# Kernel optimization log

Hardware: AMD Instinct MI355X
Metric: run time of the kernel (lower is better)

## Reference

```python
import jax, jax.numpy as jnp
import numpy as np
import math

B, L, D, H, FACTOR = 4, 2048, 256, 8, 5
DH = D // H

def setup_inputs() -> dict:
    key = jax.random.key(0)
    ks = jax.random.split(key, 12)
    s = 1.0 / math.sqrt(D)
    return {
        "q": jax.random.normal(ks[0], (B, L, D), jnp.float32),
        "k": jax.random.normal(ks[1], (B, L, D), jnp.float32),
        "v": jax.random.normal(ks[2], (B, L, D), jnp.float32),
        "Wq": jax.random.normal(ks[3], (D, D), jnp.float32) * s,
        "bq": jax.random.normal(ks[4], (D,), jnp.float32) * s,
        "Wk": jax.random.normal(ks[5], (D, D), jnp.float32) * s,
        "bk": jax.random.normal(ks[6], (D,), jnp.float32) * s,
        "Wv": jax.random.normal(ks[7], (D, D), jnp.float32) * s,
        "bv": jax.random.normal(ks[8], (D,), jnp.float32) * s,
        "Wc": jax.random.normal(ks[9], (D, D), jnp.float32) * s,
        "bc": jax.random.normal(ks[10], (D,), jnp.float32) * s,
        "index_sample": jax.random.randint(ks[11], (L,), 0, L),  # U_part = min(5*L*ceil(log1p(L)), L) = L
    }

def reference(q, k, v, Wq, bq, Wk, bk, Wv, bv, Wc, bc, index_sample):
    # projections (torch Linear: x @ W^T + b)
    qp = q @ Wq.T + bq
    kp = k @ Wk.T + bk
    vp = v @ Wv.T + bv
    # NOTE: original reshapes q with a raw view (no transpose), k/v via split()
    q4 = qp.reshape(B, H, L, DH)                       # faithful to q.view(B, H, L, dh)
    k4 = kp.reshape(B, L, H, DH).transpose(0, 2, 1, 3)
    v4 = vp.reshape(B, L, H, DH).transpose(0, 2, 1, 3)
    qf = q4.reshape(B * H, L, DH)
    kf = k4.reshape(B * H, L, DH)
    vf = v4.reshape(B * H, L, DH)
    # random K sampling (with replacement); U_part == L here
    K_sample = kf[:, index_sample, :]                  # [BH, L, dh]
    QK = jnp.einsum('bld,bud->blu', qf, K_sample)      # [BH, L, L]
    M = QK.max(axis=-1) - QK.sum(axis=-1) / L          # sparsity measure [BH, L]
    u = min(FACTOR * math.ceil(math.log1p(L)), L)      # = 40
    _, top_idx = jax.lax.top_k(-M, u)                  # topk(..., largest=False)
    Q_red = jnp.take_along_axis(qf, top_idx[:, :, None], axis=1)  # [BH, u, dh]
    scores = jnp.einsum('bud,bld->bul', Q_red, kf) / math.sqrt(DH)
    probs = jax.nn.softmax(scores, axis=-1)
    out = jnp.einsum('bul,bld->bud', probs, vf)        # [BH, u, dh]
    out = out.reshape(B, H, u, DH).transpose(0, 2, 1, 3).reshape(B, u, D)
    return out @ Wc.T + bc
```

## Files before the change

kernel.cpp:

```cpp
#include <hip/hip_runtime.h>
#include <math.h>

#define B_ 4
#define L_ 2048
#define D_ 256
#define H_ 8
#define DH_ 32
#define NH_ 32
#define U_ 40
#define LD_ 524288
#define NCH_ 16

typedef __attribute__((ext_vector_type(8))) short short8;
typedef __attribute__((ext_vector_type(4))) float floatx4;

static __device__ __forceinline__ unsigned long long ullmin_(unsigned long long a, unsigned long long b) {
    return a < b ? a : b;
}
static __device__ __forceinline__ unsigned short f2bf_rne(float x) {
    unsigned u = __float_as_uint(x);
    unsigned r = u + 0x7FFFu + ((u >> 16) & 1u);
    return (unsigned short)(r >> 16);
}
static __device__ __forceinline__ float bf2f(unsigned short h) {
    return __uint_as_float(((unsigned)h) << 16);
}

__global__ __launch_bounds__(256) void wsplit(const float* __restrict__ Wq,
                                              const float* __restrict__ Wk,
                                              const float* __restrict__ Wv,
                                              unsigned short* __restrict__ Whs,
                                              unsigned short* __restrict__ Wms,
                                              unsigned short* __restrict__ Wls) {
    const int g = blockIdx.x * 256 + threadIdx.x;
    const int mat = g >> 14;
    const int rem = g & 16383;
    const int col = rem >> 6;
    const int k4 = rem & 63;
    const float* W = (mat == 0) ? Wq : (mat == 1) ? Wk : Wv;
    const float4 x = *(const float4*)(W + (size_t)col * 256 + k4 * 4);
    float xs[4] = {x.x, x.y, x.z, x.w};
    unsigned short hv[4], mv[4], lv[4];
#pragma unroll
    for (int j = 0; j < 4; ++j) {
        hv[j] = f2bf_rne(xs[j]);
        const float e1 = xs[j] - bf2f(hv[j]);
        mv[j] = f2bf_rne(e1);
        const float e2 = e1 - bf2f(mv[j]);
        lv[j] = f2bf_rne(e2);
    }
    const int colblk = col >> 6, c64 = col & 63;
    const int jt = c64 >> 4, cin = c64 & 15;
    const int kt = k4 >> 3, g8 = k4 & 7;
    const int quad = g8 >> 1, half = g8 & 1;
    const size_t o = ((((size_t)mat * 4 + colblk) * 8 + kt) << 11) +
                     jt * 512 + (quad * 16 + cin) * 8 + half * 4;
    *(ushort4*)(Whs + o) = make_ushort4(hv[0], hv[1], hv[2], hv[3]);
    *(ushort4*)(Wms + o) = make_ushort4(mv[0], mv[1], mv[2], mv[3]);
    *(ushort4*)(Wls + o) = make_ushort4(lv[0], lv[1], lv[2], lv[3]);
}

__global__ __launch_bounds__(256) void gemm_proj(const float* __restrict__ q,
                                                 const float* __restrict__ k,
                                                 const float* __restrict__ v,
                                                 const unsigned short* __restrict__ Whs,
                                                 const unsigned short* __restrict__ Wms,
                                                 const unsigned short* __restrict__ Wls,
                                                 const float* __restrict__ bq,
                                                 const float* __restrict__ bk,
                                                 const float* __restrict__ bv,
                                                 float* __restrict__ qp,
                                                 float* __restrict__ kp,
                                                 float* __restrict__ vp) {
    const int mat = blockIdx.z;
    const float* X = (mat == 0) ? q : (mat == 1) ? k : v;
    const float* bias = (mat == 0) ? bq : (mat == 1) ? bk : bv;
    float* Y = (mat == 0) ? qp : (mat == 1) ? kp : vp;
    const bool vmat = (mat == 2);

    const int t = threadIdx.x;
    const int w = t >> 6, lane = t & 63;
    const int lq = lane & 15, quad = lane >> 4;
    const int rowBase = blockIdx.x * 64 + w * 16;
    const int colBase = blockIdx.y * 128;
    const int nseg = vmat ? 16 : 24;

    __shared__ unsigned short Bls[2][12288];

    floatx4 acc[8];
#pragma unroll
    for (int nt2 = 0; nt2 < 8; ++nt2) acc[nt2] = (floatx4){0.f, 0.f, 0.f, 0.f};

    auto gsrc = [&](int s, int kt) -> const unsigned short* {
        const int p = s >> 3, rm = s & 7, chunk = rm >> 2, jj = rm & 3;
        const unsigned short* Wp = (p == 0) ? Whs : (p == 1) ? Wms : Wls;
        return Wp + (((((size_t)mat * 4 + ((blockIdx.y << 1) | chunk)) * 8 + kt) << 11) +
                     jj * 512 + lane * 8);
    };

#pragma unroll
    for (int n = 0; n < 6; ++n) {
        const int s = w + n * 4;
        if (s < nseg)
            *(short8*)&Bls[0][s * 512 + lane * 8] = *(const short8*)gsrc(s, 0);
    }
    __syncthreads();

    for (int kt = 0; kt < 8; ++kt) {
        const int buf = kt & 1;

        short8 stg[6];
#pragma unroll
        for (int n = 0; n < 6; ++n) {
            const int s = w + n * 4;
            if (kt < 7 && s < nseg) stg[n] = *(const short8*)gsrc(s, kt + 1);
        }

        short8 Ah, Am, Al;
        {
            const float* xr = X + (size_t)(rowBase + lq) * 256 + kt * 32 + quad * 8;
            const float4 x0 = *(const float4*)xr;
            const float4 x1 = *(const float4*)(xr + 4);
            float xs[8] = {x0.x, x0.y, x0.z, x0.w, x1.x, x1.y, x1.z, x1.w};
#pragma unroll
            for (int j = 0; j < 8; ++j) {
                const unsigned short h = f2bf_rne(xs[j]);
                const float e1 = xs[j] - bf2f(h);
                const unsigned short md = f2bf_rne(e1);
                Ah[j] = (short)h;
                Am[j] = (short)md;
                if (!vmat) {
                    const float e2 = e1 - bf2f(md);
                    Al[j] = (short)f2bf_rne(e2);
                }
            }
        }

        const unsigned short* Bb = Bls[buf];
#pragma unroll
        for (int nt2 = 0; nt2 < 8; ++nt2) {
            const int boff = ((nt2 >> 2) << 11) + ((nt2 & 3) << 9) + lane * 8;
            const short8 Bh = *(const short8*)&Bb[boff];
            const short8 Bm = *(const short8*)&Bb[4096 + boff];
            floatx4 a = acc[nt2];
            if (!vmat) {
                const short8 Bl = *(const short8*)&Bb[8192 + boff];
                a = __builtin_amdgcn_mfma_f32_16x16x32_bf16(Am, Bm, a, 0, 0, 0);
                a = __builtin_amdgcn_mfma_f32_16x16x32_bf16(Ah, Bl, a, 0, 0, 0);
                a = __builtin_amdgcn_mfma_f32_16x16x32_bf16(Al, Bh, a, 0, 0, 0);
                a = __builtin_amdgcn_mfma_f32_16x16x32_bf16(Ah, Bm, a, 0, 0, 0);
                a = __builtin_amdgcn_mfma_f32_16x16x32_bf16(Am, Bh, a, 0, 0, 0);
                a = __builtin_amdgcn_mfma_f32_16x16x32_bf16(Ah, Bh, a, 0, 0, 0);
            } else {
                a = __builtin_amdgcn_mfma_f32_16x16x32_bf16(Ah, Bm, a, 0, 0, 0);
                a = __builtin_amdgcn_mfma_f32_16x16x32_bf16(Am, Bh, a, 0, 0, 0);
                a = __builtin_amdgcn_mfma_f32_16x16x32_bf16(Ah, Bh, a, 0, 0, 0);
            }
            acc[nt2] = a;
        }

#pragma unroll
        for (int n = 0; n < 6; ++n) {
            const int s = w + n * 4;
            if (kt < 7 && s < nseg)
                *(short8*)&Bls[buf ^ 1][s * 512 + lane * 8] = stg[n];
        }
        __syncthreads();
    }

#pragma unroll
    for (int nt2 = 0; nt2 < 8; ++nt2) {
        const int c = colBase + nt2 * 16 + lq;
        const float bv_ = bias[c];
#pragma unroll
        for (int r = 0; r < 4; ++r) {
            const int mr = rowBase + quad * 4 + r;
            Y[(size_t)mr * 256 + c] = acc[nt2][r] + bv_;
        }
    }
}

__global__ __launch_bounds__(256) void kconv_ksum(const float* __restrict__ kp,
                                                  const int* __restrict__ idx,
                                                  unsigned short* __restrict__ Khi,
                                                  unsigned short* __restrict__ Klo,
                                                  float* __restrict__ Ksum32) {
    const int blk = ((blockIdx.x & 7) << 7) + (blockIdx.x >> 3);
    const int i = blk >> 5, uc = blk & 31;
    const int b = i >> 3, h = i & 7;
    const int t = threadIdx.x;
    const int dq = (t & 7) * 4;
    const int ur = t >> 3;

    __shared__ float part[32][36];
    float ksum[4] = {0.f, 0.f, 0.f, 0.f};

#pragma unroll
    for (int p = 0; p < 2; ++p) {
        int u = uc * 64 + p * 32 + ur;
        const float4 x = *(const float4*)(kp + (size_t)b * LD_ + (size_t)idx[u] * D_ + h * DH_ + dq);
        float xs[4] = {x.x, x.y, x.z, x.w};
        unsigned short hv[4], lv[4];
#pragma unroll
        for (int j = 0; j < 4; ++j) {
            ksum[j] += xs[j];
            hv[j] = f2bf_rne(xs[j]);
            lv[j] = f2bf_rne(xs[j] - bf2f(hv[j]));
        }
        size_t o = ((size_t)i * 2048 + u) * 32 + dq;
        *(ushort4*)(Khi + o) = make_ushort4(hv[0], hv[1], hv[2], hv[3]);
        *(ushort4*)(Klo + o) = make_ushort4(lv[0], lv[1], lv[2], lv[3]);
    }
#pragma unroll
    for (int j = 0; j < 4; ++j) part[ur][dq + j] = ksum[j];
    __syncthreads();
    if (t < 32) {
        float s = 0.f;
#pragma unroll 8
        for (int u2 = 0; u2 < 32; ++u2) s += part[u2][t];
        Ksum32[(size_t)blk * 32 + t] = s;
    }
}

__global__ __launch_bounds__(256) void mpart_mfma(const float* __restrict__ qp,
                                                  const unsigned short* __restrict__ Khi,
                                                  const unsigned short* __restrict__ Klo,
                                                  const float* __restrict__ Ksum32,
                                                  float* __restrict__ Mv,
                                                  float* __restrict__ Qmean) {
    const int lb = ((blockIdx.x & 7) << 6) + (blockIdx.x >> 3);
    const int i = lb >> 4;
    const int lg = lb & 15;
    const int t = threadIdx.x;
    const int w = t >> 6;
    const int lane = t & 63;
    const int lq = lane & 15;
    const int quad = lane >> 4;

    __shared__ float ssum[32];
    __shared__ float red[4][128];
    if (t < 32) {
        float s = 0.f;
#pragma unroll 8
        for (int uc = 0; uc < 32; ++uc) s += Ksum32[((size_t)i * 32 + uc) * 32 + t];
        ssum[t] = s;
    }

    short8 Ah[8], Al[8];
#pragma unroll
    for (int lt = 0; lt < 8; ++lt) {
        const int l = lg * 128 + lt * 16 + lq;
        const float* qrow = qp + ((size_t)i * 2048 + l) * 32 + quad * 8;
        float4 x0 = *(const float4*)(qrow);
        float4 x1 = *(const float4*)(qrow + 4);
        float xs[8] = {x0.x, x0.y, x0.z, x0.w, x1.x, x1.y, x1.z, x1.w};
#pragma unroll
        for (int j = 0; j < 8; ++j) {
            unsigned short h = f2bf_rne(xs[j]);
            unsigned short lo = f2bf_rne(xs[j] - bf2f(h));
            Ah[lt][j] = (short)h;
            Al[lt][j] = (short)lo;
        }
    }

    floatx4 rmax[8];
#pragma unroll
    for (int lt = 0; lt < 8; ++lt)
        rmax[lt] = (floatx4){-INFINITY, -INFINITY, -INFINITY, -INFINITY};

    const size_t kfrag = ((size_t)i * 2048 + w * 512 + lq) * 32 + quad * 8;
    const unsigned short* ph = Khi + kfrag;
    const unsigned short* pl = Klo + kfrag;
#pragma unroll 2
    for (int s = 0; s < 32; ++s) {
        short8 Bh = *(const short8*)(ph + (size_t)s * 512);
        short8 Bl = *(const short8*)(pl + (size_t)s * 512);
#pragma unroll
        for (int lt = 0; lt < 8; ++lt) {
            floatx4 acc = (floatx4){0.f, 0.f, 0.f, 0.f};
            acc = __builtin_amdgcn_mfma_f32_16x16x32_bf16(Al[lt], Bh, acc, 0, 0, 0);
            acc = __builtin_amdgcn_mfma_f32_16x16x32_bf16(Ah[lt], Bl, acc, 0, 0, 0);
            acc = __builtin_amdgcn_mfma_f32_16x16x32_bf16(Ah[lt], Bh, acc, 0, 0, 0);
#pragma unroll
            for (int r = 0; r < 4; ++r) rmax[lt][r] = fmaxf(rmax[lt][r], acc[r]);
        }
    }

#pragma unroll
    for (int lt = 0; lt < 8; ++lt)
#pragma unroll
        for (int r = 0; r < 4; ++r) {
            float v = rmax[lt][r];
#pragma unroll
            for (int off = 1; off < 16; off <<= 1)
                v = fmaxf(v, __shfl_xor(v, off, 64));
            rmax[lt][r] = v;
        }
    if (lq == 0) {
#pragma unroll
        for (int lt = 0; lt < 8; ++lt)
#pragma unroll
            for (int r = 0; r < 4; ++r)
                red[w][lt * 16 + quad * 4 + r] = rmax[lt][r];
    }
    __syncthreads();
    if (t < 128) {
        const int l = lg * 128 + t;
        float m = fmaxf(fmaxf(red[0][t], red[1][t]), fmaxf(red[2][t], red[3][t]));
        const float4* q4 = (const float4*)(qp + ((size_t)i * 2048 + l) * 32);
        const float4* s4 = (const float4*)ssum;
        float qs = 0.f;
#pragma unroll
        for (int z = 0; z < 8; ++z) {
            float4 a = q4[z];
            float4 c = s4[z];
            qs = fmaf(a.x, c.x, qs);
            qs = fmaf(a.y, c.y, qs);
            qs = fmaf(a.z, c.z, qs);
            qs = fmaf(a.w, c.w, qs);
        }
        const float qm = qs * (1.0f / 2048.0f);
        Qmean[(size_t)i * 2048 + l] = qm;
        Mv[(size_t)i * 2048 + l] = m - qm;
    }
}

__global__ __launch_bounds__(256) void topk64_fast(const float* __restrict__ Mv,
                                                   int* __restrict__ candIdx) {
    const int i = blockIdx.x;
    const int t = threadIdx.x;
    const int w = t >> 6, lane = t & 63;

    __shared__ unsigned hist[256];
    __shared__ unsigned sh_prefix, sh_selBelow;
    __shared__ unsigned cnt;
    __shared__ int candLds[64];
    __shared__ unsigned long long wred[4];

    unsigned v[8];
#pragma unroll
    for (int j = 0; j < 8; ++j) {
        const unsigned u = __float_as_uint(Mv[(size_t)i * 2048 + t + 256 * j]);
        v[j] = (u & 0x80000000u) ? ~u : (u | 0x80000000u);
    }

    if (t == 0) { sh_prefix = 0u; sh_selBelow = 0u; cnt = 0u; }

    for (int level = 0; level < 4; ++level) {
        const int shift = 24 - 8 * level;
        __syncthreads();
        const unsigned prefHi = sh_prefix;
        const unsigned selB = sh_selBelow;
        const unsigned mask = (level == 0) ? 0u : (0xFFFFFFFFu << (shift + 8));
        hist[t] = 0u;
        __syncthreads();
#pragma unroll
        for (int j = 0; j < 8; ++j)
            if ((v[j] & mask) == prefHi)
                atomicAdd(&hist[(v[j] >> shift) & 255u], 1u);
        __syncthreads();
        if (t < 64) {
            const unsigned c0 = hist[t * 4 + 0], c1 = hist[t * 4 + 1];
            const unsigned c2 = hist[t * 4 + 2], c3 = hist[t * 4 + 3];
            const unsigned i0 = c0, i1 = c0 + c1, i2 = i1 + c2, i3 = i2 + c3;
            unsigned x = i3;
#pragma unroll
            for (int off = 1; off < 64; off <<= 1) {
                const unsigned y = __shfl_up(x, off, 64);
                if (t >= off) x += y;
            }
            const unsigned excl = x - i3;
            const unsigned r = 64u - selB;
            const unsigned long long ball = __ballot(x >= r);
            const int flane = __ffsll(ball) - 1;
            if (t == flane) {
                unsigned k, ce;
                if (excl + i0 >= r)      { k = 0u; ce = excl; }
                else if (excl + i1 >= r) { k = 1u; ce = excl + i0; }
                else if (excl + i2 >= r) { k = 2u; ce = excl + i1; }
                else                     { k = 3u; ce = excl + i2; }
                sh_prefix = prefHi | (((unsigned)t * 4u + k) << shift);
                sh_selBelow = selB + ce;
            }
        }
    }
    __syncthreads();
    const unsigned thr = sh_prefix;
    const unsigned selB = sh_selBelow;
    const int rem = 64 - (int)selB;

    unsigned long long keys[8];
#pragma unroll
    for (int j = 0; j < 8; ++j) {
        const int l = t + 256 * j;
        if (v[j] < thr) {
            const unsigned p = atomicAdd(&cnt, 1u);
            candLds[p] = l;
            keys[j] = ~0ULL;
        } else if (v[j] == thr) {
            keys[j] = ((unsigned long long)v[j] << 32) | (unsigned)l;
        } else {
            keys[j] = ~0ULL;
        }
    }
    __syncthreads();

    for (int it = 0; it < rem; ++it) {
        unsigned long long best = keys[0];
#pragma unroll
        for (int j = 1; j < 8; ++j) best = ullmin_(best, keys[j]);
#pragma unroll
        for (int off = 1; off < 64; off <<= 1)
            best = ullmin_(best, __shfl_xor(best, off, 64));
        if (lane == 0) wred[w] = best;
        __syncthreads();
        const unsigned long long m = ullmin_(ullmin_(wred[0], wred[1]), ullmin_(wred[2], wred[3]));
        if (t == 0) candLds[selB + it] = (int)(m & 0xffffffffu);
#pragma unroll
        for (int j = 0; j < 8; ++j)
            if (keys[j] == m) keys[j] = ~0ULL;
        __syncthreads();
    }

    if (t < 64) candIdx[i * 64 + t] = candLds[t];
}

__global__ __launch_bounds__(256) void refine_kernel(const float* __restrict__ qp,
                                                     const float* __restrict__ kp,
                                                     const int* __restrict__ idx,
                                                     const int* __restrict__ candIdx,
                                                     float* __restrict__ refPart) {
    const int blk = blockIdx.x;
    const int i = blk >> 3, c = blk & 7;
    const int b = i >> 3, h = i & 7;
    const int t = threadIdx.x;
    __shared__ float qc[64][40];
    __shared__ float Ks[128][40];

    {
        const int cand = t >> 2, dp = (t & 3) * 8;
        const int l = candIdx[i * 64 + cand];
        const float* src = qp + ((size_t)i * 2048 + l) * 32 + dp;
        *(float4*)&qc[cand][dp] = *(const float4*)(src);
        *(float4*)&qc[cand][dp + 4] = *(const float4*)(src + 4);
    }
    __syncthreads();

    const int cand = t >> 2, usub = t & 3;
    float qv[32];
#pragma unroll
    for (int z = 0; z < 8; ++z) {
        float4 a = *(const float4*)&qc[cand][z * 4];
        qv[4 * z] = a.x; qv[4 * z + 1] = a.y; qv[4 * z + 2] = a.z; qv[4 * z + 3] = a.w;
    }

    float m = -INFINITY;
    for (int s = 0; s < 2; ++s) {
        {
            const int r = t >> 1, half = t & 1;
            const int u = c * 256 + s * 128 + r;
            const float* krow = kp + (size_t)b * LD_ + (size_t)idx[u] * D_ + h * DH_ + half * 16;
#pragma unroll
            for (int z = 0; z < 4; ++z)
                *(float4*)&Ks[r][half * 16 + z * 4] = *(const float4*)(krow + z * 4);
        }
        __syncthreads();
        for (int ur = usub; ur < 128; ur += 4) {
            float a0 = 0, a1 = 0, a2 = 0, a3 = 0;
#pragma unroll
            for (int z = 0; z < 8; ++z) {
                float4 kv = *(const float4*)&Ks[ur][z * 4];
                a0 = fmaf(qv[4 * z], kv.x, a0);
                a1 = fmaf(qv[4 * z + 1], kv.y, a1);
                a2 = fmaf(qv[4 * z + 2], kv.z, a2);
                a3 = fmaf(qv[4 * z + 3], kv.w, a3);
            }
            m = fmaxf(m, (a0 + a1) + (a2 + a3));
        }
        __syncthreads();
    }
    m = fmaxf(m, __shfl_xor(m, 1, 64));
    m = fmaxf(m, __shfl_xor(m, 2, 64));
    if ((t & 3) == 0) refPart[((size_t)i * 8 + c) * 64 + cand] = m;
}

#define SCP2 136
#define VSP 36

__global__ __launch_bounds__(320) void attn_part(const float* __restrict__ qp,
                                                 const float* __restrict__ kp,
                                                 const float* __restrict__ vp,
                                                 const int* __restrict__ candIdx,
                                                 const float* __restrict__ refPart,
                                                 const float* __restrict__ Qmean,
                                                 float* __restrict__ mPart,
                                                 float* __restrict__ sPart,
                                                 float* __restrict__ oPart) {
    const int blk = blockIdx.x;
    const int i = blk >> 4, c = blk & 15;
    const int b = i >> 3, h = i & 7;
    const int t = threadIdx.x;

    __shared__ float Qs[40][32];
    __shared__ float Vs[128][VSP];
    __shared__ float sc[40][SCP2];
    __shared__ float mred[40], sred[40];
    __shared__ int topl[40];

    if (t < 64) {
        const int l = candIdx[i * 64 + t];
        float m = -INFINITY;
#pragma unroll
        for (int cc = 0; cc < 8; ++cc) m = fmaxf(m, refPart[((size_t)i * 8 + cc) * 64 + t]);
        float Mex = m - Qmean[(size_t)i * 2048 + l];
        unsigned u32 = __float_as_uint(Mex);
        u32 = (u32 & 0x80000000u) ? ~u32 : (u32 | 0x80000000u);
        unsigned long long key = ((unsigned long long)u32 << 32) | (unsigned)l;
        for (int it = 0; it < 40; ++it) {
            unsigned long long k2 = key;
#pragma unroll
            for (int off = 1; off < 64; off <<= 1) k2 = ullmin_(k2, __shfl_xor(k2, off, 64));
            if (key == k2) {
                topl[it] = l;
                key = ~0ULL;
            }
        }
    } else {
        for (int e = t - 64; e < 1024; e += 256) {
            const int r = e >> 3, qq = e & 7;
            *(float4*)&Vs[r][qq * 4] =
                *(const float4*)(vp + (size_t)b * LD_ + (size_t)(c * 128 + r) * 256 + h * 32 + qq * 4);
        }
    }
    __syncthreads();

    {
        const int r = t >> 3, qq = t & 7;
        const int lq = topl[r];
        *(float4*)&Qs[r][qq * 4] = *(const float4*)(qp + ((size_t)i * 2048 + lq) * 32 + qq * 4);
    }
    __syncthreads();

    const float scale = 0.17677669529663687f;

    if (t < 256) {
        const int r = t >> 1;
        const int j0 = (t & 1) * 20;
        const float* kr = kp + (size_t)b * LD_ + (size_t)(c * 128 + r) * 256 + h * 32;
        float kv[32];
#pragma unroll
        for (int z = 0; z < 8; ++z) {
            float4 x = *(const float4*)(kr + z * 4);
            kv[4 * z] = x.x; kv[4 * z + 1] = x.y; kv[4 * z + 2] = x.z; kv[4 * z + 3] = x.w;
        }
#pragma unroll 4
        for (int jj = 0; jj < 20; ++jj) {
            const int j = j0 + jj;
            float a0 = 0, a1 = 0, a2 = 0, a3 = 0;
#pragma unroll
            for (int z = 0; z < 8; ++z) {
                const float4 q4 = *(const float4*)&Qs[j][z * 4];
                a0 = fmaf(kv[4 * z], q4.x, a0);
                a1 = fmaf(kv[4 * z + 1], q4.y, a1);
                a2 = fmaf(kv[4 * z + 2], q4.z, a2);
                a3 = fmaf(kv[4 * z + 3], q4.w, a3);
            }
            sc[j][r] = ((a0 + a1) + (a2 + a3)) * scale;
        }
    }
    __syncthreads();

    {
        const int w = t >> 6, lane = t & 63;
#pragma unroll
        for (int rr = 0; rr < 8; ++rr) {
            const int j = w * 8 + rr;
            float x0 = sc[j][lane], x1 = sc[j][lane + 64];
            float m = fmaxf(x0, x1);
#pragma unroll
            for (int off = 1; off < 64; off <<= 1) m = fmaxf(m, __shfl_xor(m, off, 64));
            const float e0 = __expf(x0 - m), e1 = __expf(x1 - m);
            sc[j][lane] = e0; sc[j][lane + 64] = e1;
            float s = e0 + e1;
#pragma unroll
            for (int off = 1; off < 64; off <<= 1) s += __shfl_xor(s, off, 64);
            if (lane == 0) { mred[j] = m; sred[j] = s; }
        }
    }
    __syncthreads();

    {
        const int j = t >> 3, qq = t & 7;
        float4 acc = make_float4(0.f, 0.f, 0.f, 0.f);
        for (int l = 0; l < 128; ++l) {
            const float p = sc[j][l];
            const float4 v4 = *(const float4*)&Vs[l][qq * 4];
            acc.x = fmaf(p, v4.x, acc.x);
            acc.y = fmaf(p, v4.y, acc.y);
            acc.z = fmaf(p, v4.z, acc.z);
            acc.w = fmaf(p, v4.w, acc.w);
        }
        const size_t o = (size_t)(i * NCH_ + c) * 40 + j;
        *(float4*)&oPart[o * 32 + qq * 4] = acc;
        if (qq == 0) { mPart[o] = mred[j]; sPart[o] = sred[j]; }
    }
}

__global__ __launch_bounds__(256) void attn_combine(const float* __restrict__ mPart,
                                                    const float* __restrict__ sPart,
                                                    const float* __restrict__ oPart,
                                                    float* __restrict__ attnOut) {
    const int blk = blockIdx.x;
    const int b = blk / 40, j = blk - b * 40;
    const int t = threadIdx.x;
    const int h = t >> 5, d = t & 31;
    const int i = b * 8 + h;

    float mv[NCH_];
    float M = -INFINITY;
#pragma unroll
    for (int c = 0; c < NCH_; ++c) {
        mv[c] = mPart[(size_t)(i * NCH_ + c) * 40 + j];
        M = fmaxf(M, mv[c]);
    }
    float S = 0.f, O = 0.f;
#pragma unroll
    for (int c = 0; c < NCH_; ++c) {
        const float sc_ = __expf(mv[c] - M);
        const size_t o = (size_t)(i * NCH_ + c) * 40 + j;
        S = fmaf(sPart[o], sc_, S);
        O = fmaf(oPart[o * 32 + d], sc_, O);
    }
    attnOut[((size_t)b * 40 + j) * 256 + h * 32 + d] = O / S;
}

__global__ __launch_bounds__(256) void gemm_out(const float* __restrict__ X,
                                                const float* __restrict__ Wc,
                                                const float* __restrict__ bias,
                                                float* __restrict__ Y) {
    const int t = threadIdx.x;
    const int rowBase = blockIdx.x * 16;
    const int colBase = blockIdx.y * 64;
    const int col = colBase + (t & 63);
    const int rq = (t >> 6) * 4;

    __shared__ float Xs[16][256];
#pragma unroll
    for (int e = t; e < 1024; e += 256) {
        const int r = e >> 6, kq = (e & 63) * 4;
        *(float4*)&Xs[r][kq] = *(const float4*)(X + (size_t)(rowBase + r) * 256 + kq);
    }
    __syncthreads();

    const float* wr = Wc + (size_t)col * 256;
    float acc[4] = {0.f, 0.f, 0.f, 0.f};
#pragma unroll 8
    for (int k = 0; k < 256; k += 4) {
        const float4 wv = *(const float4*)(wr + k);
#pragma unroll
        for (int r = 0; r < 4; ++r) {
            acc[r] = fmaf(Xs[rq + r][k + 0], wv.x, acc[r]);
            acc[r] = fmaf(Xs[rq + r][k + 1], wv.y, acc[r]);
            acc[r] = fmaf(Xs[rq + r][k + 2], wv.z, acc[r]);
            acc[r] = fmaf(Xs[rq + r][k + 3], wv.w, acc[r]);
        }
    }

    const float bv = bias[col];
#pragma unroll
    for (int r = 0; r < 4; ++r)
        Y[(size_t)(rowBase + rq + r) * 256 + col] = acc[r] + bv;
}

extern "C" void kernel_launch(void* const* d_in, const int* in_sizes, int n_in,
                              void* d_out, int out_size, void* d_ws, size_t ws_size,
                              hipStream_t stream) {
    const float* q  = (const float*)d_in[0];
    const float* k  = (const float*)d_in[1];
    const float* v  = (const float*)d_in[2];
    const float* Wq = (const float*)d_in[3];
    const float* bq = (const float*)d_in[4];
    const float* Wk = (const float*)d_in[5];
    const float* bk = (const float*)d_in[6];
    const float* Wv = (const float*)d_in[7];
    const float* bv = (const float*)d_in[8];
    const float* Wc = (const float*)d_in[9];
    const float* bc = (const float*)d_in[10];
    const int* idx  = (const int*)d_in[11];
    float* out = (float*)d_out;

    char* w = (char*)d_ws;
    float*          qp      = (float*)(w);
    float*          kp      = (float*)(w + (8u << 20));
    float*          vp      = (float*)(w + (16u << 20));
    unsigned short* Khi     = (unsigned short*)(w + (24u << 20));
    unsigned short* Klo     = (unsigned short*)(w + (28u << 20));
    float*          Mv      = (float*)(w + (32u << 20));
    float*          Qmean   = (float*)(w + (32u << 20) + (256u << 10));
    float*          Ksum32  = (float*)(w + (32u << 20) + (512u << 10));
    int*            candIdx = (int*)  (w + (32u << 20) + (640u << 10));
    float*          refPart = (float*)(w + (32u << 20) + (656u << 10));
    float*          attnOut = (float*)(w + (32u << 20) + (720u << 10));
    unsigned short* Whs     = (unsigned short*)(w + (40u << 20));
    unsigned short* Wms     = (unsigned short*)(w + (40u << 20) + (512u << 10));
    unsigned short* Wls     = (unsigned short*)(w + (41u << 20));
    float*          mPart   = (float*)(w + (24u << 20));
    float*          sPart   = (float*)(w + (24u << 20) + (128u << 10));
    float*          oPart   = (float*)(w + (24u << 20) + (256u << 10));

    hipLaunchKernelGGL(wsplit, dim3(192), dim3(256), 0, stream, Wq, Wk, Wv, Whs, Wms, Wls);
    hipLaunchKernelGGL(gemm_proj, dim3(128, 2, 3), dim3(256), 0, stream,
                       q, k, v, Whs, Wms, Wls, bq, bk, bv, qp, kp, vp);
    hipLaunchKernelGGL(kconv_ksum, dim3(1024), dim3(256), 0, stream, kp, idx, Khi, Klo, Ksum32);
    hipLaunchKernelGGL(mpart_mfma, dim3(512), dim3(256), 0, stream, qp, Khi, Klo, Ksum32, Mv, Qmean);
    hipLaunchKernelGGL(topk64_fast, dim3(32), dim3(256), 0, stream, Mv, candIdx);
    hipLaunchKernelGGL(refine_kernel, dim3(256), dim3(256), 0, stream, qp, kp, idx, candIdx, refPart);
    hipLaunchKernelGGL(attn_part, dim3(512), dim3(320), 0, stream,
                       qp, kp, vp, candIdx, refPart, Qmean, mPart, sPart, oPart);
    hipLaunchKernelGGL(attn_combine, dim3(160), dim3(256), 0, stream, mPart, sPart, oPart, attnOut);
    hipLaunchKernelGGL(gemm_out, dim3(10, 4), dim3(256), 0, stream, attnOut, Wc, bc, out);
}
```

Measured before the change: 213.7 us.

## Pre-split activations into bf16 hi/mid/lo tiles in a separate kernel

Adds an xsplit kernel that converts q/k/v into three bf16 components stored in an MFMA-fragment-friendly tiled layout. gemm_proj then loads these fragments directly and register-prefetches the next k-tile instead of converting fp32 inline, which removes the split arithmetic from the GEMM's critical path. The cost is an extra launch and roughly 1.5x the original activation bytes written and re-read through global memory (the three bf16 planes, with no lo plane for v), plus a larger workspace.

```diff
diff --git a/kernel.cpp b/kernel.cpp
--- a/kernel.cpp
+++ b/kernel.cpp
@@ -60,9 +60,43 @@
     *(ushort4*)(Wls + o) = make_ushort4(lv[0], lv[1], lv[2], lv[3]);
 }
 
-__global__ __launch_bounds__(256) void gemm_proj(const float* __restrict__ q,
-                                                 const float* __restrict__ k,
-                                                 const float* __restrict__ v,
+__global__ __launch_bounds__(256) void xsplit(const float* __restrict__ q,
+                                              const float* __restrict__ k,
+                                              const float* __restrict__ v,
+                                              unsigned short* __restrict__ Xh,
+                                              unsigned short* __restrict__ Xm,
+                                              unsigned short* __restrict__ Xl) {
+    const int g = blockIdx.x * 256 + threadIdx.x;
+    const int mat = g >> 19;
+    const int rem = g & 524287;
+    const int row = rem >> 6;
+    const int k4 = rem & 63;
+    const float* X = (mat == 0) ? q : (mat == 1) ? k : v;
+    const float4 x = *(const float4*)(X + (size_t)row * 256 + k4 * 4);
+    float xs[4] = {x.x, x.y, x.z, x.w};
+    unsigned short hv[4], mv[4], lv[4];
+#pragma unroll
+    for (int j = 0; j < 4; ++j) {
+        hv[j] = f2bf_rne(xs[j]);
+        const float e1 = xs[j] - bf2f(hv[j]);
+        mv[j] = f2bf_rne(e1);
+        const float e2 = e1 - bf2f(mv[j]);
+        lv[j] = f2bf_rne(e2);
+    }
+    const int rowtile = row >> 4, rin = row & 15;
+    const int kt = k4 >> 3, g8 = k4 & 7;
+    const int quad = g8 >> 1, half = g8 & 1;
+    const size_t o = ((((size_t)mat * 512 + rowtile) * 8 + kt) << 9) +
+                     (quad * 16 + rin) * 8 + half * 4;
+    *(ushort4*)(Xh + o) = make_ushort4(hv[0], hv[1], hv[2], hv[3]);
+    *(ushort4*)(Xm + o) = make_ushort4(mv[0], mv[1], mv[2], mv[3]);
+    if (mat < 2)
+        *(ushort4*)(Xl + o) = make_ushort4(lv[0], lv[1], lv[2], lv[3]);
+}
+
+__global__ __launch_bounds__(256) void gemm_proj(const unsigned short* __restrict__ Xh,
+                                                 const unsigned short* __restrict__ Xm,
+                                                 const unsigned short* __restrict__ Xl,
                                                  const unsigned short* __restrict__ Whs,
                                                  const unsigned short* __restrict__ Wms,
                                                  const unsigned short* __restrict__ Wls,
@@ -73,7 +107,6 @@
                                                  float* __restrict__ kp,
                                                  float* __restrict__ vp) {
     const int mat = blockIdx.z;
-    const float* X = (mat == 0) ? q : (mat == 1) ? k : v;
     const float* bias = (mat == 0) ? bq : (mat == 1) ? bk : bv;
     float* Y = (mat == 0) ? qp : (mat == 1) ? kp : vp;
     const bool vmat = (mat == 2);
@@ -84,6 +117,7 @@
     const int rowBase = blockIdx.x * 64 + w * 16;
     const int colBase = blockIdx.y * 128;
     const int nseg = vmat ? 16 : 24;
+    const int rowtile = blockIdx.x * 4 + w;
 
     __shared__ unsigned short Bls[2][12288];
 
@@ -97,6 +131,9 @@
         return Wp + (((((size_t)mat * 4 + ((blockIdx.y << 1) | chunk)) * 8 + kt) << 11) +
                      jj * 512 + lane * 8);
     };
+    auto abase = [&](int kt) -> size_t {
+        return ((((size_t)mat * 512 + rowtile) * 8 + kt) << 9) + lane * 8;
+    };
 
 #pragma unroll
     for (int n = 0; n < 6; ++n) {
@@ -104,35 +141,25 @@
         if (s < nseg)
             *(short8*)&Bls[0][s * 512 + lane * 8] = *(const short8*)gsrc(s, 0);
     }
+    short8 Ah = *(const short8*)(Xh + abase(0));
+    short8 Am = *(const short8*)(Xm + abase(0));
+    short8 Al;
+    if (!vmat) Al = *(const short8*)(Xl + abase(0));
     __syncthreads();
 
     for (int kt = 0; kt < 8; ++kt) {
         const int buf = kt & 1;
 
+        short8 nAh, nAm, nAl;
         short8 stg[6];
-#pragma unroll
-        for (int n = 0; n < 6; ++n) {
-            const int s = w + n * 4;
-            if (kt < 7 && s < nseg) stg[n] = *(const short8*)gsrc(s, kt + 1);
-        }
-
-        short8 Ah, Am, Al;
-        {
-            const float* xr = X + (size_t)(rowBase + lq) * 256 + kt * 32 + quad * 8;
-            const float4 x0 = *(const float4*)xr;
-            const float4 x1 = *(const float4*)(xr + 4);
-            float xs[8] = {x0.x, x0.y, x0.z, x0.w, x1.x, x1.y, x1.z, x1.w};
-#pragma unroll
-            for (int j = 0; j < 8; ++j) {
-                const unsigned short h = f2bf_rne(xs[j]);
-                const float e1 = xs[j] - bf2f(h);
-                const unsigned short md = f2bf_rne(e1);
-                Ah[j] = (short)h;
-                Am[j] = (short)md;
-                if (!vmat) {
-                    const float e2 = e1 - bf2f(md);
-                    Al[j] = (short)f2bf_rne(e2);
-                }
+        if (kt < 7) {
+            nAh = *(const short8*)(Xh + abase(kt + 1));
+            nAm = *(const short8*)(Xm + abase(kt + 1));
+            if (!vmat) nAl = *(const short8*)(Xl + abase(kt + 1));
+#pragma unroll
+            for (int n = 0; n < 6; ++n) {
+                const int s = w + n * 4;
+                if (s < nseg) stg[n] = *(const short8*)gsrc(s, kt + 1);
             }
         }
 
@@ -165,6 +192,8 @@
             if (kt < 7 && s < nseg)
                 *(short8*)&Bls[buf ^ 1][s * 512 + lane * 8] = stg[n];
         }
+        Ah = nAh; Am = nAm;
+        if (!vmat) Al = nAl;
         __syncthreads();
     }
 
@@ -693,6 +722,9 @@
     float*          qp      = (float*)(w);
     float*          kp      = (float*)(w + (8u << 20));
     float*          vp      = (float*)(w + (16u << 20));
+    unsigned short* Xh      = (unsigned short*)(w + (24u << 20));
+    unsigned short* Xm      = (unsigned short*)(w + (36u << 20));
+    unsigned short* Xl      = (unsigned short*)(w + (48u << 20));
     unsigned short* Khi     = (unsigned short*)(w + (24u << 20));
     unsigned short* Klo     = (unsigned short*)(w + (28u << 20));
     float*          Mv      = (float*)(w + (32u << 20));
@@ -701,16 +733,17 @@
     int*            candIdx = (int*)  (w + (32u << 20) + (640u << 10));
     float*          refPart = (float*)(w + (32u << 20) + (656u << 10));
     float*          attnOut = (float*)(w + (32u << 20) + (720u << 10));
-    unsigned short* Whs     = (unsigned short*)(w + (40u << 20));
-    unsigned short* Wms     = (unsigned short*)(w + (40u << 20) + (512u << 10));
-    unsigned short* Wls     = (unsigned short*)(w + (41u << 20));
+    unsigned short* Whs     = (unsigned short*)(w + (56u << 20));
+    unsigned short* Wms     = (unsigned short*)(w + (56u << 20) + (512u << 10));
+    unsigned short* Wls     = (unsigned short*)(w + (57u << 20));
     float*          mPart   = (float*)(w + (24u << 20));
     float*          sPart   = (float*)(w + (24u << 20) + (128u << 10));
     float*          oPart   = (float*)(w + (24u << 20) + (256u << 10));
 
     hipLaunchKernelGGL(wsplit, dim3(192), dim3(256), 0, stream, Wq, Wk, Wv, Whs, Wms, Wls);
+    hipLaunchKernelGGL(xsplit, dim3(6144), dim3(256), 0, stream, q, k, v, Xh, Xm, Xl);
     hipLaunchKernelGGL(gemm_proj, dim3(128, 2, 3), dim3(256), 0, stream,
-                       q, k, v, Whs, Wms, Wls, bq, bk, bv, qp, kp, vp);
+                       Xh, Xm, Xl, Whs, Wms, Wls, bq, bk, bv, qp, kp, vp);
     hipLaunchKernelGGL(kconv_ksum, dim3(1024), dim3(256), 0, stream, kp, idx, Khi, Klo, Ksum32);
     hipLaunchKernelGGL(mpart_mfma, dim3(512), dim3(256), 0, stream, qp, Khi, Klo, Ksum32, Mv, Qmean);
     hipLaunchKernelGGL(topk64_fast, dim3(32), dim3(256), 0, stream, Mv, candIdx);
```

Result: slower. 239.7 us (+12.1%).
